# Optimization experiments

Hardware: AMD Instinct MI355X
Metric: run time of the kernel (lower is better)

Reference implementation:

```python
import jax, jax.numpy as jnp
import numpy as np

EPS = 1e-8
NUM_HEADS = 8
SCALE = 25.0
SIM_THRESH = 0.75
BLOCK = 10  # per-frame proposal group size used by the zeroing mask


def _l2norm(x):
    return x / (jnp.linalg.norm(x, axis=-1, keepdims=True) + EPS)


def setup_inputs() -> dict:
    key = jax.random.key(0)
    ks = jax.random.split(key, 7)
    B, N, C = 1, 2000, 256
    H = NUM_HEADS
    x_cls = jax.random.normal(ks[0], (B, N, C), dtype=jnp.float32)
    x_reg = jax.random.normal(ks[1], (B, N, C), dtype=jnp.float32)
    cls_score = jax.random.uniform(ks[2], (N,), dtype=jnp.float32)
    fg_score = jax.random.uniform(ks[3], (N,), dtype=jnp.float32)
    coord_attn = jax.random.uniform(ks[4], (B, H, N, N), dtype=jnp.float32)
    W_qkv_cls = jax.random.normal(ks[5], (3 * C, C), dtype=jnp.float32) * 0.02
    W_qkv_reg = jax.random.normal(ks[6], (3 * C, C), dtype=jnp.float32) * 0.02
    return {"x_cls": x_cls, "x_reg": x_reg, "cls_score": cls_score,
            "fg_score": fg_score, "coord_attn": coord_attn,
            "W_qkv_cls": W_qkv_cls, "W_qkv_reg": W_qkv_reg}


def reference(x_cls, x_reg, cls_score, fg_score, coord_attn, W_qkv_cls, W_qkv_reg):
    B, N, C = x_cls.shape
    H = NUM_HEADS
    D = C // H

    def qkv(x, W):
        t = (x @ W.T).reshape(B, N, 3, H, D).transpose(2, 0, 3, 1, 4)  # [3,B,H,N,D]
        return t[0], t[1], t[2]

    q_cls, k_cls, v_cls = qkv(x_cls, W_qkv_cls)
    q_reg, k_reg, v_reg = qkv(x_reg, W_qkv_reg)

    q_cls, k_cls = _l2norm(q_cls), _l2norm(k_cls)
    q_reg, k_reg = _l2norm(q_reg), _l2norm(k_reg)
    v_cls_normed = _l2norm(v_cls)

    cs = cls_score.reshape(1, 1, 1, N)  # broadcast over [B,H,N,N]
    fs = fg_score.reshape(1, 1, 1, N)

    attn_cls_raw = jnp.einsum('bhnd,bhmd->bhnm', v_cls_normed, v_cls_normed)

    attn_cls = jax.nn.softmax(jnp.einsum('bhnd,bhmd->bhnm', q_cls, k_cls) * SCALE * cs, axis=-1)
    attn_reg = jax.nn.softmax(jnp.einsum('bhnd,bhmd->bhnm', q_reg, k_reg) * SCALE * fs, axis=-1)

    attn = (attn_reg + attn_cls) * 0.5 * coord_attn
    attn = jax.lax.stop_gradient(attn)  # original detaches before masking

    # block-diagonal zeroing: row j zeros cols [j//10*10, j//10*10+9), keep diagonal
    rows = jnp.arange(N)[:, None]
    cols = jnp.arange(N)[None, :]
    block_start = (rows // BLOCK) * BLOCK
    zero_mask = (cols >= block_start) & (cols < block_start + (BLOCK - 1)) & (cols != rows)
    attn = jnp.where(zero_mask, 0.0, attn)

    x = jnp.einsum('bhnm,bhmd->bhnd', attn, v_cls).transpose(0, 2, 1, 3).reshape(B, N, C)
    x_ori = v_cls.transpose(0, 2, 1, 3).reshape(B, N, C)
    x_cat = jnp.concatenate([x, x_ori], axis=-1)  # [B,N,2C]

    # ave=True branch
    sim_raw = jnp.sum(attn_cls_raw, axis=1)[0] / H          # [N,N]
    sim_mask = (sim_raw > SIM_THRESH).astype(x_cls.dtype)
    sim_attn = jnp.sum(attn, axis=1)[0] / H                 # [N,N]
    sim_round2 = jax.nn.softmax(sim_attn, axis=-1)
    sim_round2 = sim_mask * sim_round2 / (jnp.sum(sim_mask * sim_round2, axis=-1, keepdims=True) + EPS)
    return x_cat, sim_round2
```

## Files before the change

### kernel.cpp

```cpp
#include <hip/hip_runtime.h>
#include <math.h>

typedef _Float16 half8 __attribute__((ext_vector_type(8)));
typedef _Float16 half4 __attribute__((ext_vector_type(4)));
typedef _Float16 half2v __attribute__((ext_vector_type(2)));
typedef float f32x4 __attribute__((ext_vector_type(4)));

constexpr int N = 2000;
constexpr int NP = 2048;
constexpr int H = 8;
constexpr int D = 32;
constexpr float SCL = 25.0f;
constexpr float L2E = 1.4426950408889634f;
constexpr float FM2 = 25.0f * L2E;

#define MFMA16(a,b,c)  __builtin_amdgcn_mfma_f32_16x16x32_f16((a),(b),(c),0,0,0)
#define MFMA16K(a,b,c) __builtin_amdgcn_mfma_f32_16x16x16f16((a),(b),(c),0,0,0)

__device__ __forceinline__ float fexp2(float x) { return __builtin_amdgcn_exp2f(x); }


__global__ __launch_bounds__(256) void wconv_kernel(
    const float* __restrict__ Wc, const float* __restrict__ Wr,
    _Float16* __restrict__ Wch, _Float16* __restrict__ Wrh)
{
    const int i = blockIdx.x * 256 + threadIdx.x;
    Wch[i] = (_Float16)Wc[i];
    Wrh[i] = (_Float16)Wr[i];
}

__global__ __launch_bounds__(256) void qkv_kernel(
    const float* __restrict__ xc, const float* __restrict__ xr,
    const _Float16* __restrict__ Wch, const _Float16* __restrict__ Wrh,
    const float* __restrict__ clsScore, const float* __restrict__ fgScore,
    _Float16* __restrict__ Qch, _Float16* __restrict__ Kch,
    _Float16* __restrict__ Qrh, _Float16* __restrict__ Krh,
    _Float16* __restrict__ Vnh, _Float16* __restrict__ Vth,
    float* __restrict__ out)
{
    constexpr int XS = 264;
    __shared__ _Float16 xs[16 * XS];
    const int t = threadIdx.x;
    const int n0 = blockIdx.x * 16;
    const int by = blockIdx.y;
    const int which = (by < 3) ? by : (by - 3);
    const bool isCls = by < 3;
    const float* x = isCls ? xc : xr;
    const _Float16* Wh = isCls ? Wch : Wrh;

    #pragma unroll
    for (int it = 0; it < 4; ++it) {
        const int f = t + it * 256;
        const int row = f >> 6, c4 = f & 63;
        const float4 v = *(const float4*)(x + (size_t)(n0 + row) * 256 + c4 * 4);
        half4 hv; hv[0]=(_Float16)v.x; hv[1]=(_Float16)v.y; hv[2]=(_Float16)v.z; hv[3]=(_Float16)v.w;
        *(half4*)&xs[row * XS + c4 * 4] = hv;
    }
    __syncthreads();

    const int w = t >> 6, l = t & 63;
    const int lr = l & 15, lg = l >> 4;
    const int obase = which * 256 + w * 64;
    f32x4 acc[4] = {{0,0,0,0},{0,0,0,0},{0,0,0,0},{0,0,0,0}};
    for (int k0 = 0; k0 < 256; k0 += 32) {
        const half8 aX = *(const half8*)&xs[lr * XS + k0 + lg * 8];
        #pragma unroll
        for (int s = 0; s < 4; ++s) {
            const half8 bW = *(const half8*)(Wh + (size_t)(obase + s * 16 + lr) * 256 + k0 + lg * 8);
            acc[s] = MFMA16(aX, bW, acc[s]);
        }
    }
    f32x4 kscale = {1.f,1.f,1.f,1.f};
    if (which == 1) {
        const float* sp = isCls ? clsScore : fgScore;
        kscale = (SCL * L2E) * *(const f32x4*)(sp + n0 + lg*4);
    }
    #pragma unroll
    for (int p = 0; p < 2; ++p) {
        const int h = 2 * w + p;
        float ss[4];
        #pragma unroll
        for (int j = 0; j < 4; ++j) {
            float v = acc[2*p][j]*acc[2*p][j] + acc[2*p+1][j]*acc[2*p+1][j];
            #pragma unroll
            for (int off = 1; off < 16; off <<= 1) v += __shfl_xor(v, off);
            ss[j] = sqrtf(v) + 1e-8f;
        }
        if (which < 2) {
            _Float16* Qd = isCls ? (which == 0 ? Qch : Kch) : (which == 0 ? Qrh : Krh);
            #pragma unroll
            for (int sh = 0; sh < 2; ++sh)
                #pragma unroll
                for (int j = 0; j < 4; ++j)
                    Qd[((size_t)h*NP + n0 + lg*4 + j)*D + sh*16 + lr]
                        = (_Float16)(acc[2*p+sh][j] / ss[j] * kscale[j]);
        } else {
            #pragma unroll
            for (int sh = 0; sh < 2; ++sh) {
                const int d = sh * 16 + lr;
                half4 tv;
                #pragma unroll
                for (int j = 0; j < 4; ++j) {
                    const float raw = acc[2*p+sh][j];
                    Vnh[((size_t)h*NP + n0 + lg*4 + j)*D + d] = (_Float16)(raw / ss[j]);
                    out[(size_t)(n0 + lg*4 + j)*512 + 256 + h*D + d] = raw;
                    tv[j] = (_Float16)raw;
                }
                *(half4*)(Vth + ((size_t)h*D + d)*NP + n0 + lg*4) = tv;
            }
        }
    }
}

__global__ __launch_bounds__(512) void stats_kernel(
    const _Float16* __restrict__ Qch, const _Float16* __restrict__ Kch,
    const _Float16* __restrict__ Qrh, const _Float16* __restrict__ Krh,
    float* __restrict__ BIAS)
{
    __shared__ float Ssh[2][4][16];
    const int t = threadIdx.x;
    const int w = t >> 6, l = t & 63;
    const int nsub = w >> 2, mq = w & 3;
    const int n0 = blockIdx.x * 32 + nsub * 16;
    const int h = blockIdx.y, z = blockIdx.z;
    const _Float16* Q = z ? Qrh : Qch;
    const _Float16* K = z ? Krh : Kch;
    const int lr = l & 15, lg = l >> 4;
    const half8 aQ = *(const half8*)(Q + ((size_t)h*NP + n0 + lr)*D + lg*8);
    float S[4] = {0.f, 0.f, 0.f, 0.f};
    const int mqB0 = (mq == 0) ? 0 : 31*mq;
    const int mqB1 = (mq == 3) ? 125 : 31*(mq+1);
    half8 bK = *(const half8*)(K + ((size_t)h*NP + mqB0*16 + lr)*D + lg*8);
    for (int ms = mqB0; ms < mqB1; ++ms) {
        const half8 cur = bK;
        if (ms + 1 < mqB1)
            bK = *(const half8*)(K + ((size_t)h*NP + (ms+1)*16 + lr)*D + lg*8);
        f32x4 z4 = {0.f, 0.f, 0.f, 0.f};
        const f32x4 c = MFMA16(aQ, cur, z4);
        #pragma unroll
        for (int j = 0; j < 4; ++j) S[j] += fexp2(c[j] - FM2);
    }
    #pragma unroll
    for (int j = 0; j < 4; ++j) {
        #pragma unroll
        for (int off = 1; off < 16; off <<= 1) S[j] += __shfl_xor(S[j], off);
    }
    if (lr == 0) {
        #pragma unroll
        for (int j = 0; j < 4; ++j) Ssh[nsub][mq][lg*4 + j] = S[j];
    }
    __syncthreads();
    if (t < 32) {
        const int ns = t >> 4, rl = t & 15;
        const int n = blockIdx.x * 32 + ns*16 + rl;
        BIAS[((size_t)z*H + h)*NP + n]
            = -__log2f(Ssh[ns][0][rl] + Ssh[ns][1][rl] + Ssh[ns][2][rl] + Ssh[ns][3][rl]) - FM2 - 1.0f;
    }
}

__global__ __launch_bounds__(256) void vvmask_kernel(
    const _Float16* __restrict__ Vnh, unsigned char* __restrict__ Mask)
{
    const int t = threadIdx.x;
    const int w = t >> 6, l = t & 63;
    const int n0 = blockIdx.y * 16;
    const int m00 = blockIdx.x * 256 + w * 64;
    const int lr = l & 15, lg = l >> 4;
    half8 aV[8];
    #pragma unroll
    for (int h = 0; h < 8; ++h)
        aV[h] = *(const half8*)(Vnh + ((size_t)(h*NP + n0 + lr))*D + lg*8);
    for (int s = 0; s < 4; ++s) {
        const int mb = m00 + s*16;
        f32x4 acc = {0.f, 0.f, 0.f, 0.f};
        #pragma unroll
        for (int h = 0; h < 8; ++h) {
            const half8 bV = *(const half8*)(Vnh + ((size_t)(h*NP + mb + lr))*D + lg*8);
            acc = MFMA16(aV[h], bV, acc);
        }
        const int m = mb + lr;
        if (m < N) {
            #pragma unroll
            for (int j = 0; j < 4; ++j) {
                const int n = n0 + lg*4 + j;
                Mask[(size_t)n*N + m] = (acc[j]*0.125f > 0.75f) ? (unsigned char)1 : (unsigned char)0;
            }
        }
    }
}

template<int SMAX>
__global__ __launch_bounds__(256) void attn_kernel(
    const _Float16* __restrict__ Kch, const _Float16* __restrict__ Krh,
    const _Float16* __restrict__ Qch, const _Float16* __restrict__ Qrh,
    const _Float16* __restrict__ Vth, const float* __restrict__ coord,
    const float* __restrict__ BIAS,
    _Float16* __restrict__ SIMH, _Float16* __restrict__ XPH, int mcBase)
{
    __shared__ _Float16 simred[4][16][SMAX*16 + 8];

    const int t = threadIdx.x;
    const int w = t >> 6, l = t & 63;
    const int lr = l & 15, lg = l >> 4;
    const int mc = mcBase + blockIdx.x;
    const int m0 = mc * 128;
    const int n0 = blockIdx.y * 16;
    const int n = n0 + lr;
    const int bs = (n / 10) * 10;
    const int h0 = 2 * w;

    unsigned kill = 0u;
    #pragma unroll
    for (int s = 0; s < SMAX; ++s)
        #pragma unroll
        for (int j = 0; j < 4; ++j) {
            const int m = m0 + s*16 + lg*4 + j;
            if (m >= bs && m < bs + 9 && m != n) kill |= (1u << (s*4 + j));
        }

    half2v sacc[SMAX][2];
    #pragma unroll
    for (int s = 0; s < SMAX; ++s)
        #pragma unroll
        for (int k = 0; k < 2; ++k) { sacc[s][k][0] = (_Float16)0.f; sacc[s][k][1] = (_Float16)0.f; }

    constexpr int NG = (SMAX + 3) / 4;

    #pragma unroll
    for (int hp = 0; hp < 2; ++hp) {
        const int h = h0 + hp;
        const half8 aQc = *(const half8*)(Qch + ((size_t)h*NP + n)*D + lg*8);
        const half8 aQr = *(const half8*)(Qrh + ((size_t)h*NP + n)*D + lg*8);
        const float bC = BIAS[(size_t)h*NP + n];
        const float bR = BIAS[(size_t)(H + h)*NP + n];
        f32x4 pv0 = {0,0,0,0}, pv1 = {0,0,0,0};

        #pragma unroll
        for (int g = 0; g < NG; ++g) {
            constexpr int GSfull = 4;
            const int gs = (SMAX - 4*g >= 4) ? GSfull : (SMAX - 4*g);
            half8 kc[4], kr[4]; half4 v0[4], v1[4]; f32x4 co[4];
            #pragma unroll
            for (int i = 0; i < 4; ++i) {
                if (i >= gs) break;
                const int s = 4*g + i;
                const int m = m0 + s*16;
                const size_t kb = ((size_t)h*NP + m + lr)*D + lg*8;
                kc[i] = *(const half8*)(Kch + kb);
                kr[i] = *(const half8*)(Krh + kb);
                v0[i] = *(const half4*)(Vth + ((size_t)(h*D + lr))*NP + m + lg*4);
                v1[i] = *(const half4*)(Vth + ((size_t)(h*D + 16 + lr))*NP + m + lg*4);
                co[i] = *(const f32x4*)(coord + ((size_t)h*N + n)*N + m + lg*4);
            }
            __builtin_amdgcn_sched_barrier(0);
            #pragma unroll
            for (int i = 0; i < 4; ++i) {
                if (i >= gs) break;
                const int s = 4*g + i;
                f32x4 z4 = {0,0,0,0};
                const f32x4 cc = MFMA16(kc[i], aQc, z4);
                const f32x4 cr = MFMA16(kr[i], aQr, z4);
                half4 af;
                #pragma unroll
                for (int j = 0; j < 4; ++j) {
                    float a = (fexp2(cc[j] + bC) + fexp2(cr[j] + bR)) * co[i][j];
                    if ((kill >> (s*4 + j)) & 1u) a = 0.f;
                    af[j] = (_Float16)a;
                }
                sacc[s][0] += (half2v){af[0], af[1]};
                sacc[s][1] += (half2v){af[2], af[3]};
                pv0 = MFMA16K(af, v0[i], pv0);
                pv1 = MFMA16K(af, v1[i], pv1);
            }
            __builtin_amdgcn_sched_barrier(0);
        }
        _Float16* xp = XPH + (((size_t)(mc*H + h)*N + n0 + lg*4))*D + lr;
        #pragma unroll
        for (int j = 0; j < 4; ++j) {
            xp[j*D]      = (_Float16)pv0[j];
            xp[j*D + 16] = (_Float16)pv1[j];
        }
    }

    #pragma unroll
    for (int s = 0; s < SMAX; ++s) {
        half4 sv; sv[0]=sacc[s][0][0]; sv[1]=sacc[s][0][1]; sv[2]=sacc[s][1][0]; sv[3]=sacc[s][1][1];
        *(half4*)&simred[w][lr][s*16 + lg*4] = sv;
    }
    __syncthreads();
    constexpr int C8 = SMAX * 2;
    for (int e = t; e < 16 * C8; e += 256) {
        const int r = e / C8, c8 = e % C8;
        const half8 s0 = *(const half8*)&simred[0][r][c8*8];
        const half8 s1 = *(const half8*)&simred[1][r][c8*8];
        const half8 s2 = *(const half8*)&simred[2][r][c8*8];
        const half8 s3 = *(const half8*)&simred[3][r][c8*8];
        const half8 sum = (s0 + s1) + (s2 + s3);
        *(half8*)(SIMH + (size_t)(n0 + r)*N + m0 + c8*8) = sum;
    }
}

__global__ __launch_bounds__(256) void reduce_kernel(
    const _Float16* __restrict__ XPH, float* __restrict__ out)
{
    const int n = blockIdx.x, t = threadIdx.x;
    const int h = t >> 5, d = t & 31;
    float acc = 0.f;
    #pragma unroll
    for (int mcI = 0; mcI < 16; ++mcI)
        acc += (float)XPH[(((size_t)mcI*H + h)*N + n)*D + d];
    out[(size_t)n*512 + t] = acc;
}

__global__ __launch_bounds__(256) void simfinal_kernel(
    const _Float16* __restrict__ SIMH, const unsigned char* __restrict__ Mask,
    float* __restrict__ out)
{
    __shared__ float redA[4], redB[4];
    const int n = blockIdx.x, t = threadIdx.x;
    const _Float16* row = SIMH + (size_t)n * N;
    const unsigned char* mrow = Mask + (size_t)n * N;
    const bool act = t < 250;
    float f[8];
    unsigned int mk0 = 0, mk1 = 0;
    float mx = -1e30f;
    if (act) {
        const half8 v8 = *(const half8*)(row + t*8);
        const uint2 mm = *(const uint2*)(mrow + t*8);
        mk0 = mm.x; mk1 = mm.y;
        #pragma unroll
        for (int k = 0; k < 8; ++k) { f[k] = (float)v8[k]; mx = fmaxf(mx, f[k]); }
    }
    #pragma unroll
    for (int off = 1; off < 64; off <<= 1) mx = fmaxf(mx, __shfl_xor(mx, off));
    const int wv = t >> 6;
    if ((t & 63) == 0) redA[wv] = mx;
    __syncthreads();
    const float M = fmaxf(fmaxf(redA[0], redA[1]), fmaxf(redA[2], redA[3]));
    float e[8];
    float sA = 0.f, sM = 0.f;
    if (act) {
        #pragma unroll
        for (int k = 0; k < 8; ++k) {
            e[k] = fexp2((f[k] - M) * (L2E * 0.125f));
            sA += e[k];
            const unsigned int mkb = ((k < 4 ? mk0 : mk1) >> (8*(k & 3))) & 0xffu;
            if (mkb) sM += e[k]; else e[k] = 0.f;
        }
    }
    #pragma unroll
    for (int off = 1; off < 64; off <<= 1) { sA += __shfl_xor(sA, off); sM += __shfl_xor(sM, off); }
    __syncthreads();
    if ((t & 63) == 0) { redA[wv] = sA; redB[wv] = sM; }
    __syncthreads();
    const float SA = redA[0] + redA[1] + redA[2] + redA[3];
    const float SMK = redB[0] + redB[1] + redB[2] + redB[3];
    const float inv = 1.f / (SMK + 1e-8f * SA);
    if (act) {
        float* orow = out + 1024000 + (size_t)n*N + t*8;
        *(float4*)(orow)     = make_float4(e[0]*inv, e[1]*inv, e[2]*inv, e[3]*inv);
        *(float4*)(orow + 4) = make_float4(e[4]*inv, e[5]*inv, e[6]*inv, e[7]*inv);
    }
}

extern "C" void kernel_launch(void* const* d_in, const int* in_sizes, int n_in,
                              void* d_out, int out_size, void* d_ws, size_t ws_size,
                              hipStream_t stream) {
    const float* x_cls     = (const float*)d_in[0];
    const float* x_reg     = (const float*)d_in[1];
    const float* cls_score = (const float*)d_in[2];
    const float* fg_score  = (const float*)d_in[3];
    const float* coord     = (const float*)d_in[4];
    const float* Wc        = (const float*)d_in[5];
    const float* Wr        = (const float*)d_in[6];

    char* base = (char*)d_ws;
    float* BIAS     = (float*)base;
    _Float16* SIMH  = (_Float16*)(base + 131072);
    _Float16* XPH   = (_Float16*)(base + 8131072);
    _Float16* Qch   = (_Float16*)(base + 24515072);
    _Float16* Kch   = Qch + 524288;
    _Float16* Qrh   = Qch + 2*524288;
    _Float16* Krh   = Qch + 3*524288;
    _Float16* Vnh   = Qch + 4*524288;
    _Float16* Vth   = Qch + 5*524288;
    _Float16* Wch   = (_Float16*)(base + 30806528);
    _Float16* Wrh   = (_Float16*)(base + 31199744);
    unsigned char* Mask = (unsigned char*)(base + 31592960);
    float* out = (float*)d_out;

    wconv_kernel<<<768, 256, 0, stream>>>(Wc, Wr, Wch, Wrh);
    qkv_kernel<<<dim3(125, 5), 256, 0, stream>>>(x_cls, x_reg, Wch, Wrh, cls_score, fg_score,
                                                 Qch, Kch, Qrh, Krh, Vnh, Vth, out);
    stats_kernel<<<dim3(63, 8, 2), 512, 0, stream>>>(Qch, Kch, Qrh, Krh, BIAS);
    vvmask_kernel<<<dim3(8, 125), 256, 0, stream>>>(Vnh, Mask);
    attn_kernel<8><<<dim3(15, 125), 256, 0, stream>>>(Kch, Krh, Qch, Qrh, Vth, coord,
                                                      BIAS, SIMH, XPH, 0);
    attn_kernel<5><<<dim3(1, 125), 256, 0, stream>>>(Kch, Krh, Qch, Qrh, Vth, coord,
                                                     BIAS, SIMH, XPH, 15);
    reduce_kernel<<<2000, 256, 0, stream>>>(XPH, out);
    simfinal_kernel<<<2000, 256, 0, stream>>>(SIMH, Mask, out);
}
```

Measured before the change: 135.2 us.

## Prepack coord attention into fp16 MFMA-fragment layout before attention

Adds a kernel that converts the coord_attn tensor to fp16 and stores it tiled in the exact per-lane fragment order used by the attention kernel. The attention kernel then loads contiguous half4 values instead of strided fp32 rows, aiming to improve coalescing and halve bytes in the hot loop. This adds an extra full pass over the large coord tensor plus a 64MB intermediate write and read, and reduces coord precision to fp16.

```diff
diff --git a/kernel.cpp b/kernel.cpp
--- a/kernel.cpp
+++ b/kernel.cpp
@@ -27,6 +27,35 @@
     const int i = blockIdx.x * 256 + threadIdx.x;
     Wch[i] = (_Float16)Wc[i];
     Wrh[i] = (_Float16)Wr[i];
+}
+
+__global__ __launch_bounds__(256) void pack_kernel(
+    const float* __restrict__ coord, _Float16* __restrict__ CH)
+{
+    const int ny = blockIdx.x, h = blockIdx.y;
+    const int t = threadIdx.x;
+    const int row = t >> 4;
+    const int c0 = (t & 15) * 4;
+    const float* src = coord + ((size_t)h*N + ny*16 + row)*N;
+    _Float16* dstbase = CH + ((size_t)(h*125 + ny))*125*256;
+    const int lp = ((t & 3) << 4) | row;
+    #pragma unroll 8
+    for (int k = 0; k < 31; ++k) {
+        const int colb = c0 + 64*k;
+        const f32x4 v = *(const f32x4*)(src + colb);
+        const int ms = colb >> 4;
+        half4 hv; hv[0]=(_Float16)v[0]; hv[1]=(_Float16)v[1]; hv[2]=(_Float16)v[2]; hv[3]=(_Float16)v[3];
+        *(half4*)(dstbase + ((size_t)ms*64 + lp)*4) = hv;
+    }
+    {
+        const int colb = c0 + 64*31;
+        if (colb < 2000) {
+            const f32x4 v = *(const f32x4*)(src + colb);
+            const int ms = colb >> 4;
+            half4 hv; hv[0]=(_Float16)v[0]; hv[1]=(_Float16)v[1]; hv[2]=(_Float16)v[2]; hv[3]=(_Float16)v[3];
+            *(half4*)(dstbase + ((size_t)ms*64 + lp)*4) = hv;
+        }
+    }
 }
 
 __global__ __launch_bounds__(256) void qkv_kernel(
@@ -193,7 +222,7 @@
 __global__ __launch_bounds__(256) void attn_kernel(
     const _Float16* __restrict__ Kch, const _Float16* __restrict__ Krh,
     const _Float16* __restrict__ Qch, const _Float16* __restrict__ Qrh,
-    const _Float16* __restrict__ Vth, const float* __restrict__ coord,
+    const _Float16* __restrict__ Vth, const _Float16* __restrict__ CH,
     const float* __restrict__ BIAS,
     _Float16* __restrict__ SIMH, _Float16* __restrict__ XPH, int mcBase)
 {
@@ -203,8 +232,9 @@
     const int w = t >> 6, l = t & 63;
     const int lr = l & 15, lg = l >> 4;
     const int mc = mcBase + blockIdx.x;
+    const int ny = blockIdx.y;
     const int m0 = mc * 128;
-    const int n0 = blockIdx.y * 16;
+    const int n0 = ny * 16;
     const int n = n0 + lr;
     const int bs = (n / 10) * 10;
     const int h0 = 2 * w;
@@ -233,13 +263,14 @@
         const half8 aQr = *(const half8*)(Qrh + ((size_t)h*NP + n)*D + lg*8);
         const float bC = BIAS[(size_t)h*NP + n];
         const float bR = BIAS[(size_t)(H + h)*NP + n];
+        const _Float16* chh = CH + ((size_t)(h*125 + ny)*125 + mc*8)*256;
         f32x4 pv0 = {0,0,0,0}, pv1 = {0,0,0,0};
 
         #pragma unroll
         for (int g = 0; g < NG; ++g) {
             constexpr int GSfull = 4;
             const int gs = (SMAX - 4*g >= 4) ? GSfull : (SMAX - 4*g);
-            half8 kc[4], kr[4]; half4 v0[4], v1[4]; f32x4 co[4];
+            half8 kc[4], kr[4]; half4 v0[4], v1[4], co[4];
             #pragma unroll
             for (int i = 0; i < 4; ++i) {
                 if (i >= gs) break;
@@ -250,7 +281,7 @@
                 kr[i] = *(const half8*)(Krh + kb);
                 v0[i] = *(const half4*)(Vth + ((size_t)(h*D + lr))*NP + m + lg*4);
                 v1[i] = *(const half4*)(Vth + ((size_t)(h*D + 16 + lr))*NP + m + lg*4);
-                co[i] = *(const f32x4*)(coord + ((size_t)h*N + n)*N + m + lg*4);
+                co[i] = *(const half4*)(chh + s*256 + l*4);
             }
             __builtin_amdgcn_sched_barrier(0);
             #pragma unroll
@@ -263,7 +294,7 @@
                 half4 af;
                 #pragma unroll
                 for (int j = 0; j < 4; ++j) {
-                    float a = (fexp2(cc[j] + bC) + fexp2(cr[j] + bR)) * co[i][j];
+                    float a = (fexp2(cc[j] + bC) + fexp2(cr[j] + bR)) * (float)co[i][j];
                     if ((kill >> (s*4 + j)) & 1u) a = 0.f;
                     af[j] = (_Float16)a;
                 }
@@ -387,16 +418,18 @@
     _Float16* Wch   = (_Float16*)(base + 30806528);
     _Float16* Wrh   = (_Float16*)(base + 31199744);
     unsigned char* Mask = (unsigned char*)(base + 31592960);
+    _Float16* CH    = (_Float16*)(base + 35592960);
     float* out = (float*)d_out;
 
     wconv_kernel<<<768, 256, 0, stream>>>(Wc, Wr, Wch, Wrh);
+    pack_kernel<<<dim3(125, 8), 256, 0, stream>>>(coord, CH);
     qkv_kernel<<<dim3(125, 5), 256, 0, stream>>>(x_cls, x_reg, Wch, Wrh, cls_score, fg_score,
                                                  Qch, Kch, Qrh, Krh, Vnh, Vth, out);
     stats_kernel<<<dim3(63, 8, 2), 512, 0, stream>>>(Qch, Kch, Qrh, Krh, BIAS);
     vvmask_kernel<<<dim3(8, 125), 256, 0, stream>>>(Vnh, Mask);
-    attn_kernel<8><<<dim3(15, 125), 256, 0, stream>>>(Kch, Krh, Qch, Qrh, Vth, coord,
+    attn_kernel<8><<<dim3(15, 125), 256, 0, stream>>>(Kch, Krh, Qch, Qrh, Vth, CH,
                                                       BIAS, SIMH, XPH, 0);
-    attn_kernel<5><<<dim3(1, 125), 256, 0, stream>>>(Kch, Krh, Qch, Qrh, Vth, coord,
+    attn_kernel<5><<<dim3(1, 125), 256, 0, stream>>>(Kch, Krh, Qch, Qrh, Vth, CH,
                                                      BIAS, SIMH, XPH, 15);
     reduce_kernel<<<2000, 256, 0, stream>>>(XPH, out);
     simfinal_kernel<<<2000, 256, 0, stream>>>(SIMH, Mask, out);
```

New measurement: 159.1 us. 17.8% more time.

## Split fused attention into score, coord-stream, and PV kernels via fp16 buffer

Applied to the files above, without the earlier changes.

The fused attention kernel is split into three passes. The first computes exp scores into an fp16 [H,N,N] buffer. The second streams coord_attn with that buffer, applies the block mask, writes the masked probabilities back and produces the head-summed similarity. The third runs the P·V matmul per head and writes the output directly, which removes the per-chunk partial buffer and its reduce kernel. This makes the coord read fully coalesced and separates the memory-bound and compute-bound work. The cost is writing and re-reading a 64 MB fp16 intermediate twice more.

```diff
diff --git a/kernel.cpp b/kernel.cpp
--- a/kernel.cpp
+++ b/kernel.cpp
@@ -3,7 +3,6 @@
 
 typedef _Float16 half8 __attribute__((ext_vector_type(8)));
 typedef _Float16 half4 __attribute__((ext_vector_type(4)));
-typedef _Float16 half2v __attribute__((ext_vector_type(2)));
 typedef float f32x4 __attribute__((ext_vector_type(4)));
 
 constexpr int N = 2000;
@@ -190,15 +189,11 @@
 }
 
 template<int SMAX>
-__global__ __launch_bounds__(256) void attn_kernel(
+__global__ __launch_bounds__(256) void escore_kernel(
     const _Float16* __restrict__ Kch, const _Float16* __restrict__ Krh,
     const _Float16* __restrict__ Qch, const _Float16* __restrict__ Qrh,
-    const _Float16* __restrict__ Vth, const float* __restrict__ coord,
-    const float* __restrict__ BIAS,
-    _Float16* __restrict__ SIMH, _Float16* __restrict__ XPH, int mcBase)
-{
-    __shared__ _Float16 simred[4][16][SMAX*16 + 8];
-
+    const float* __restrict__ BIAS, _Float16* __restrict__ EP, int mcBase)
+{
     const int t = threadIdx.x;
     const int w = t >> 6, l = t & 63;
     const int lr = l & 15, lg = l >> 4;
@@ -206,23 +201,7 @@
     const int m0 = mc * 128;
     const int n0 = blockIdx.y * 16;
     const int n = n0 + lr;
-    const int bs = (n / 10) * 10;
     const int h0 = 2 * w;
-
-    unsigned kill = 0u;
-    #pragma unroll
-    for (int s = 0; s < SMAX; ++s)
-        #pragma unroll
-        for (int j = 0; j < 4; ++j) {
-            const int m = m0 + s*16 + lg*4 + j;
-            if (m >= bs && m < bs + 9 && m != n) kill |= (1u << (s*4 + j));
-        }
-
-    half2v sacc[SMAX][2];
-    #pragma unroll
-    for (int s = 0; s < SMAX; ++s)
-        #pragma unroll
-        for (int k = 0; k < 2; ++k) { sacc[s][k][0] = (_Float16)0.f; sacc[s][k][1] = (_Float16)0.f; }
 
     constexpr int NG = (SMAX + 3) / 4;
 
@@ -233,24 +212,19 @@
         const half8 aQr = *(const half8*)(Qrh + ((size_t)h*NP + n)*D + lg*8);
         const float bC = BIAS[(size_t)h*NP + n];
         const float bR = BIAS[(size_t)(H + h)*NP + n];
-        f32x4 pv0 = {0,0,0,0}, pv1 = {0,0,0,0};
+        _Float16* erow = EP + ((size_t)h*N + n)*N;
 
         #pragma unroll
         for (int g = 0; g < NG; ++g) {
-            constexpr int GSfull = 4;
-            const int gs = (SMAX - 4*g >= 4) ? GSfull : (SMAX - 4*g);
-            half8 kc[4], kr[4]; half4 v0[4], v1[4]; f32x4 co[4];
+            const int gs = (SMAX - 4*g >= 4) ? 4 : (SMAX - 4*g);
+            half8 kc[4], kr[4];
             #pragma unroll
             for (int i = 0; i < 4; ++i) {
                 if (i >= gs) break;
                 const int s = 4*g + i;
-                const int m = m0 + s*16;
-                const size_t kb = ((size_t)h*NP + m + lr)*D + lg*8;
+                const size_t kb = ((size_t)h*NP + m0 + s*16 + lr)*D + lg*8;
                 kc[i] = *(const half8*)(Kch + kb);
                 kr[i] = *(const half8*)(Krh + kb);
-                v0[i] = *(const half4*)(Vth + ((size_t)(h*D + lr))*NP + m + lg*4);
-                v1[i] = *(const half4*)(Vth + ((size_t)(h*D + 16 + lr))*NP + m + lg*4);
-                co[i] = *(const f32x4*)(coord + ((size_t)h*N + n)*N + m + lg*4);
             }
             __builtin_amdgcn_sched_barrier(0);
             #pragma unroll
@@ -260,56 +234,106 @@
                 f32x4 z4 = {0,0,0,0};
                 const f32x4 cc = MFMA16(kc[i], aQc, z4);
                 const f32x4 cr = MFMA16(kr[i], aQr, z4);
-                half4 af;
+                half4 ev;
                 #pragma unroll
-                for (int j = 0; j < 4; ++j) {
-                    float a = (fexp2(cc[j] + bC) + fexp2(cr[j] + bR)) * co[i][j];
-                    if ((kill >> (s*4 + j)) & 1u) a = 0.f;
-                    af[j] = (_Float16)a;
-                }
-                sacc[s][0] += (half2v){af[0], af[1]};
-                sacc[s][1] += (half2v){af[2], af[3]};
-                pv0 = MFMA16K(af, v0[i], pv0);
-                pv1 = MFMA16K(af, v1[i], pv1);
+                for (int j = 0; j < 4; ++j)
+                    ev[j] = (_Float16)(fexp2(cc[j] + bC) + fexp2(cr[j] + bR));
+                *(half4*)(erow + m0 + s*16 + lg*4) = ev;
             }
-            __builtin_amdgcn_sched_barrier(0);
-        }
-        _Float16* xp = XPH + (((size_t)(mc*H + h)*N + n0 + lg*4))*D + lr;
-        #pragma unroll
-        for (int j = 0; j < 4; ++j) {
-            xp[j*D]      = (_Float16)pv0[j];
-            xp[j*D + 16] = (_Float16)pv1[j];
-        }
-    }
-
-    #pragma unroll
-    for (int s = 0; s < SMAX; ++s) {
-        half4 sv; sv[0]=sacc[s][0][0]; sv[1]=sacc[s][0][1]; sv[2]=sacc[s][1][0]; sv[3]=sacc[s][1][1];
-        *(half4*)&simred[w][lr][s*16 + lg*4] = sv;
-    }
-    __syncthreads();
-    constexpr int C8 = SMAX * 2;
-    for (int e = t; e < 16 * C8; e += 256) {
-        const int r = e / C8, c8 = e % C8;
-        const half8 s0 = *(const half8*)&simred[0][r][c8*8];
-        const half8 s1 = *(const half8*)&simred[1][r][c8*8];
-        const half8 s2 = *(const half8*)&simred[2][r][c8*8];
-        const half8 s3 = *(const half8*)&simred[3][r][c8*8];
-        const half8 sum = (s0 + s1) + (s2 + s3);
-        *(half8*)(SIMH + (size_t)(n0 + r)*N + m0 + c8*8) = sum;
-    }
-}
-
-__global__ __launch_bounds__(256) void reduce_kernel(
-    const _Float16* __restrict__ XPH, float* __restrict__ out)
-{
-    const int n = blockIdx.x, t = threadIdx.x;
-    const int h = t >> 5, d = t & 31;
-    float acc = 0.f;
-    #pragma unroll
-    for (int mcI = 0; mcI < 16; ++mcI)
-        acc += (float)XPH[(((size_t)mcI*H + h)*N + n)*D + d];
-    out[(size_t)n*512 + t] = acc;
+        }
+    }
+}
+
+__global__ __launch_bounds__(256) void stream_kernel(
+    const float* __restrict__ coord, _Float16* __restrict__ EP,
+    _Float16* __restrict__ SIMH)
+{
+    constexpr int GTOT = N * (N / 4);
+    for (int g = blockIdx.x * 256 + threadIdx.x; g < GTOT; g += gridDim.x * 256) {
+        const int n = g / (N / 4);
+        const int m = (g - n * (N / 4)) * 4;
+        const int bs = (n / 10) * 10;
+        f32x4 s4 = {0.f, 0.f, 0.f, 0.f};
+        #pragma unroll
+        for (int h = 0; h < 8; ++h) {
+            const size_t off = ((size_t)h*N + n)*N + m;
+            const f32x4 co = *(const f32x4*)(coord + off);
+            const half4 e = *(const half4*)(EP + off);
+            half4 p;
+            #pragma unroll
+            for (int j = 0; j < 4; ++j) {
+                const int mm = m + j;
+                float a = (float)e[j] * co[j];
+                if (mm >= bs && mm < bs + 9 && mm != n) a = 0.f;
+                p[j] = (_Float16)a;
+                s4[j] += a;
+            }
+            *(half4*)(EP + off) = p;
+        }
+        half4 sv;
+        #pragma unroll
+        for (int j = 0; j < 4; ++j) sv[j] = (_Float16)s4[j];
+        *(half4*)(SIMH + (size_t)n*N + m) = sv;
+    }
+}
+
+__global__ __launch_bounds__(256) void pv_kernel(
+    const _Float16* __restrict__ EP, const _Float16* __restrict__ Vth,
+    float* __restrict__ out)
+{
+    __shared__ _Float16 pvred[4][2][16][18];
+    const int t = threadIdx.x;
+    const int w = t >> 6, l = t & 63;
+    const int lr = l & 15, lg = l >> 4;
+    const int n0 = blockIdx.x * 16;
+    const int h  = blockIdx.y;
+    const int n  = n0 + lr;
+
+    const _Float16* prow = EP + ((size_t)h*N + n)*N;
+    const _Float16* v0row = Vth + ((size_t)(h*D + lr))*NP;
+    const _Float16* v1row = Vth + ((size_t)(h*D + 16 + lr))*NP;
+
+    f32x4 aA0 = {0,0,0,0}, aA1 = {0,0,0,0}, aB0 = {0,0,0,0}, aB1 = {0,0,0,0};
+    for (int ms = w; ms < 125; ms += 8) {
+        const int m1 = ms*16;
+        const int ms2 = ms + 4;
+        const half4 afA = *(const half4*)(prow + m1 + lg*4);
+        const half4 v0A = *(const half4*)(v0row + m1 + lg*4);
+        const half4 v1A = *(const half4*)(v1row + m1 + lg*4);
+        half4 afB{}, v0B{}, v1B{};
+        if (ms2 < 125) {
+            const int m2 = ms2*16;
+            afB = *(const half4*)(prow + m2 + lg*4);
+            v0B = *(const half4*)(v0row + m2 + lg*4);
+            v1B = *(const half4*)(v1row + m2 + lg*4);
+        }
+        __builtin_amdgcn_sched_barrier(0);
+        aA0 = MFMA16K(afA, v0A, aA0);
+        aA1 = MFMA16K(afA, v1A, aA1);
+        if (ms2 < 125) {
+            aB0 = MFMA16K(afB, v0B, aB0);
+            aB1 = MFMA16K(afB, v1B, aB1);
+        }
+    }
+    const f32x4 pv0 = aA0 + aB0;
+    const f32x4 pv1 = aA1 + aB1;
+    {
+        half4 h0v, h1v;
+        #pragma unroll
+        for (int j = 0; j < 4; ++j) { h0v[j] = (_Float16)pv0[j]; h1v[j] = (_Float16)pv1[j]; }
+        *(half4*)&pvred[w][0][lr][lg*4] = h0v;
+        *(half4*)&pvred[w][1][lr][lg*4] = h1v;
+    }
+    __syncthreads();
+    {
+        const int e0 = 2*t;
+        const int d = e0 & 15, db = (e0 >> 4) & 1, q = e0 >> 5;
+        const float u0 = (float)pvred[0][db][d][q]   + (float)pvred[1][db][d][q]
+                       + (float)pvred[2][db][d][q]   + (float)pvred[3][db][d][q];
+        const float u1 = (float)pvred[0][db][d+1][q] + (float)pvred[1][db][d+1][q]
+                       + (float)pvred[2][db][d+1][q] + (float)pvred[3][db][d+1][q];
+        *(float2*)(out + (size_t)(n0 + q)*512 + h*32 + db*16 + d) = make_float2(u0, u1);
+    }
 }
 
 __global__ __launch_bounds__(256) void simfinal_kernel(
@@ -377,16 +401,16 @@
     char* base = (char*)d_ws;
     float* BIAS     = (float*)base;
     _Float16* SIMH  = (_Float16*)(base + 131072);
-    _Float16* XPH   = (_Float16*)(base + 8131072);
-    _Float16* Qch   = (_Float16*)(base + 24515072);
+    _Float16* EP    = (_Float16*)(base + 8131072);
+    _Float16* Qch   = (_Float16*)(base + 72131072);
     _Float16* Kch   = Qch + 524288;
     _Float16* Qrh   = Qch + 2*524288;
     _Float16* Krh   = Qch + 3*524288;
     _Float16* Vnh   = Qch + 4*524288;
     _Float16* Vth   = Qch + 5*524288;
-    _Float16* Wch   = (_Float16*)(base + 30806528);
-    _Float16* Wrh   = (_Float16*)(base + 31199744);
-    unsigned char* Mask = (unsigned char*)(base + 31592960);
+    _Float16* Wch   = (_Float16*)(base + 78422528);
+    _Float16* Wrh   = (_Float16*)(base + 78815744);
+    unsigned char* Mask = (unsigned char*)(base + 79208960);
     float* out = (float*)d_out;
 
     wconv_kernel<<<768, 256, 0, stream>>>(Wc, Wr, Wch, Wrh);
@@ -394,10 +418,9 @@
                                                  Qch, Kch, Qrh, Krh, Vnh, Vth, out);
     stats_kernel<<<dim3(63, 8, 2), 512, 0, stream>>>(Qch, Kch, Qrh, Krh, BIAS);
     vvmask_kernel<<<dim3(8, 125), 256, 0, stream>>>(Vnh, Mask);
-    attn_kernel<8><<<dim3(15, 125), 256, 0, stream>>>(Kch, Krh, Qch, Qrh, Vth, coord,
-                                                      BIAS, SIMH, XPH, 0);
-    attn_kernel<5><<<dim3(1, 125), 256, 0, stream>>>(Kch, Krh, Qch, Qrh, Vth, coord,
-                                                     BIAS, SIMH, XPH, 15);
-    reduce_kernel<<<2000, 256, 0, stream>>>(XPH, out);
+    escore_kernel<8><<<dim3(15, 125), 256, 0, stream>>>(Kch, Krh, Qch, Qrh, BIAS, EP, 0);
+    escore_kernel<5><<<dim3(1, 125), 256, 0, stream>>>(Kch, Krh, Qch, Qrh, BIAS, EP, 15);
+    stream_kernel<<<2048, 256, 0, stream>>>(coord, EP, SIMH);
+    pv_kernel<<<dim3(125, 8), 256, 0, stream>>>(EP, Vth, out);
     simfinal_kernel<<<2000, 256, 0, stream>>>(SIMH, Mask, out);
 }
```

Measured after the change: 165.8 us. 22.7% more time.

## Restructure attention to one block per head and row tile, staging coord in LDS

Applied to the files above, without the earlier changes.

The attention kernel now assigns one block per (head, 16-row tile) and loops over all 2000 columns, so partial PV results are reduced inside the block through LDS. This removes the XPH partial buffer and the separate reduce kernel. The coord tile is prefetched into double-buffered shared memory for coalesced loads. The per-head attention weights are no longer summed across heads in registers; each head writes its own fp16 slice to an 8x larger SIM buffer that simfinal then sums. This trades the cross-head reduction for a much larger global write and read, and the launch grid shrinks to 1000 blocks.

```diff
diff --git a/kernel.cpp b/kernel.cpp
--- a/kernel.cpp
+++ b/kernel.cpp
@@ -3,7 +3,6 @@
 
 typedef _Float16 half8 __attribute__((ext_vector_type(8)));
 typedef _Float16 half4 __attribute__((ext_vector_type(4)));
-typedef _Float16 half2v __attribute__((ext_vector_type(2)));
 typedef float f32x4 __attribute__((ext_vector_type(4)));
 
 constexpr int N = 2000;
@@ -189,147 +188,146 @@
     }
 }
 
-template<int SMAX>
 __global__ __launch_bounds__(256) void attn_kernel(
     const _Float16* __restrict__ Kch, const _Float16* __restrict__ Krh,
     const _Float16* __restrict__ Qch, const _Float16* __restrict__ Qrh,
     const _Float16* __restrict__ Vth, const float* __restrict__ coord,
     const float* __restrict__ BIAS,
-    _Float16* __restrict__ SIMH, _Float16* __restrict__ XPH, int mcBase)
-{
-    __shared__ _Float16 simred[4][16][SMAX*16 + 8];
+    _Float16* __restrict__ SIMH8, float* __restrict__ out)
+{
+    constexpr int CW = 264;
+    __shared__ float costage[2][16][CW];
+    __shared__ float pvred[4][2][16][17];
 
     const int t = threadIdx.x;
     const int w = t >> 6, l = t & 63;
     const int lr = l & 15, lg = l >> 4;
-    const int mc = mcBase + blockIdx.x;
-    const int m0 = mc * 128;
-    const int n0 = blockIdx.y * 16;
-    const int n = n0 + lr;
+    const int h  = blockIdx.x;
+    const int ny = blockIdx.y;
+    const int n0 = ny * 16;
+    const int n  = n0 + lr;
     const int bs = (n / 10) * 10;
-    const int h0 = 2 * w;
-
-    unsigned kill = 0u;
-    #pragma unroll
-    for (int s = 0; s < SMAX; ++s)
-        #pragma unroll
-        for (int j = 0; j < 4; ++j) {
-            const int m = m0 + s*16 + lg*4 + j;
-            if (m >= bs && m < bs + 9 && m != n) kill |= (1u << (s*4 + j));
-        }
-
-    half2v sacc[SMAX][2];
-    #pragma unroll
-    for (int s = 0; s < SMAX; ++s)
-        #pragma unroll
-        for (int k = 0; k < 2; ++k) { sacc[s][k][0] = (_Float16)0.f; sacc[s][k][1] = (_Float16)0.f; }
-
-    constexpr int NG = (SMAX + 3) / 4;
-
-    #pragma unroll
-    for (int hp = 0; hp < 2; ++hp) {
-        const int h = h0 + hp;
-        const half8 aQc = *(const half8*)(Qch + ((size_t)h*NP + n)*D + lg*8);
-        const half8 aQr = *(const half8*)(Qrh + ((size_t)h*NP + n)*D + lg*8);
-        const float bC = BIAS[(size_t)h*NP + n];
-        const float bR = BIAS[(size_t)(H + h)*NP + n];
-        f32x4 pv0 = {0,0,0,0}, pv1 = {0,0,0,0};
-
-        #pragma unroll
-        for (int g = 0; g < NG; ++g) {
-            constexpr int GSfull = 4;
-            const int gs = (SMAX - 4*g >= 4) ? GSfull : (SMAX - 4*g);
-            half8 kc[4], kr[4]; half4 v0[4], v1[4]; f32x4 co[4];
-            #pragma unroll
-            for (int i = 0; i < 4; ++i) {
-                if (i >= gs) break;
-                const int s = 4*g + i;
-                const int m = m0 + s*16;
-                const size_t kb = ((size_t)h*NP + m + lr)*D + lg*8;
-                kc[i] = *(const half8*)(Kch + kb);
-                kr[i] = *(const half8*)(Krh + kb);
-                v0[i] = *(const half4*)(Vth + ((size_t)(h*D + lr))*NP + m + lg*4);
-                v1[i] = *(const half4*)(Vth + ((size_t)(h*D + 16 + lr))*NP + m + lg*4);
-                co[i] = *(const f32x4*)(coord + ((size_t)h*N + n)*N + m + lg*4);
+
+    const half8 aQc = *(const half8*)(Qch + ((size_t)h*NP + n)*D + lg*8);
+    const half8 aQr = *(const half8*)(Qrh + ((size_t)h*NP + n)*D + lg*8);
+    const float bC = BIAS[(size_t)h*NP + n];
+    const float bR = BIAS[(size_t)(H + h)*NP + n];
+
+    f32x4 streg[4];
+    auto LOADCH = [&](int c) {
+        #pragma unroll
+        for (int i = 0; i < 4; ++i) {
+            const int g = t + 256*i;
+            const int row = g >> 6, c4 = g & 63;
+            const int col = c*256 + c4*4;
+            if (col < 2000)
+                streg[i] = *(const f32x4*)(coord + ((size_t)h*N + n0 + row)*N + col);
+            else
+                streg[i] = (f32x4){0.f,0.f,0.f,0.f};
+        }
+    };
+    auto WRITECH = [&](int buf) {
+        #pragma unroll
+        for (int i = 0; i < 4; ++i) {
+            const int g = t + 256*i;
+            const int row = g >> 6, c4 = g & 63;
+            *(f32x4*)&costage[buf][row][c4*4] = streg[i];
+        }
+    };
+
+    f32x4 pv0 = {0,0,0,0}, pv1 = {0,0,0,0};
+
+    LOADCH(0);
+    WRITECH(0);
+    __syncthreads();
+    int buf = 0;
+
+    for (int c = 0; c < 8; ++c) {
+        const bool more = (c + 1 < 8);
+        if (more) LOADCH(c + 1);
+        __builtin_amdgcn_sched_barrier(0);
+
+        const int nls = (c < 7) ? 4 : ((w < 3) ? 4 : 1);
+
+        half8 kc[4], kr[4]; half4 v0[4], v1[4];
+        #pragma unroll
+        for (int i = 0; i < 4; ++i) {
+            if (i >= nls) break;
+            const int s = c*16 + w*4 + i;
+            const int m = s*16;
+            const size_t kb = ((size_t)h*NP + m + lr)*D + lg*8;
+            kc[i] = *(const half8*)(Kch + kb);
+            kr[i] = *(const half8*)(Krh + kb);
+            v0[i] = *(const half4*)(Vth + ((size_t)(h*D + lr))*NP + m + lg*4);
+            v1[i] = *(const half4*)(Vth + ((size_t)(h*D + 16 + lr))*NP + m + lg*4);
+        }
+        __builtin_amdgcn_sched_barrier(0);
+
+        #pragma unroll
+        for (int i = 0; i < 4; ++i) {
+            if (i >= nls) break;
+            const int s = c*16 + w*4 + i;
+            const f32x4 co = *(const f32x4*)&costage[buf][lr][(w*4 + i)*16 + lg*4];
+            f32x4 z4 = {0,0,0,0};
+            const f32x4 cc = MFMA16(kc[i], aQc, z4);
+            const f32x4 cr = MFMA16(kr[i], aQr, z4);
+            half4 af;
+            #pragma unroll
+            for (int j = 0; j < 4; ++j) {
+                const int m = s*16 + lg*4 + j;
+                float a = (fexp2(cc[j] + bC) + fexp2(cr[j] + bR)) * co[j];
+                if (m >= bs && m < bs + 9 && m != n) a = 0.f;
+                af[j] = (_Float16)a;
             }
-            __builtin_amdgcn_sched_barrier(0);
-            #pragma unroll
-            for (int i = 0; i < 4; ++i) {
-                if (i >= gs) break;
-                const int s = 4*g + i;
-                f32x4 z4 = {0,0,0,0};
-                const f32x4 cc = MFMA16(kc[i], aQc, z4);
-                const f32x4 cr = MFMA16(kr[i], aQr, z4);
-                half4 af;
-                #pragma unroll
-                for (int j = 0; j < 4; ++j) {
-                    float a = (fexp2(cc[j] + bC) + fexp2(cr[j] + bR)) * co[i][j];
-                    if ((kill >> (s*4 + j)) & 1u) a = 0.f;
-                    af[j] = (_Float16)a;
-                }
-                sacc[s][0] += (half2v){af[0], af[1]};
-                sacc[s][1] += (half2v){af[2], af[3]};
-                pv0 = MFMA16K(af, v0[i], pv0);
-                pv1 = MFMA16K(af, v1[i], pv1);
-            }
-            __builtin_amdgcn_sched_barrier(0);
-        }
-        _Float16* xp = XPH + (((size_t)(mc*H + h)*N + n0 + lg*4))*D + lr;
-        #pragma unroll
-        for (int j = 0; j < 4; ++j) {
-            xp[j*D]      = (_Float16)pv0[j];
-            xp[j*D + 16] = (_Float16)pv1[j];
-        }
-    }
-
-    #pragma unroll
-    for (int s = 0; s < SMAX; ++s) {
-        half4 sv; sv[0]=sacc[s][0][0]; sv[1]=sacc[s][0][1]; sv[2]=sacc[s][1][0]; sv[3]=sacc[s][1][1];
-        *(half4*)&simred[w][lr][s*16 + lg*4] = sv;
-    }
-    __syncthreads();
-    constexpr int C8 = SMAX * 2;
-    for (int e = t; e < 16 * C8; e += 256) {
-        const int r = e / C8, c8 = e % C8;
-        const half8 s0 = *(const half8*)&simred[0][r][c8*8];
-        const half8 s1 = *(const half8*)&simred[1][r][c8*8];
-        const half8 s2 = *(const half8*)&simred[2][r][c8*8];
-        const half8 s3 = *(const half8*)&simred[3][r][c8*8];
-        const half8 sum = (s0 + s1) + (s2 + s3);
-        *(half8*)(SIMH + (size_t)(n0 + r)*N + m0 + c8*8) = sum;
-    }
-}
-
-__global__ __launch_bounds__(256) void reduce_kernel(
-    const _Float16* __restrict__ XPH, float* __restrict__ out)
-{
-    const int n = blockIdx.x, t = threadIdx.x;
-    const int h = t >> 5, d = t & 31;
-    float acc = 0.f;
-    #pragma unroll
-    for (int mcI = 0; mcI < 16; ++mcI)
-        acc += (float)XPH[(((size_t)mcI*H + h)*N + n)*D + d];
-    out[(size_t)n*512 + t] = acc;
+            *(half4*)(SIMH8 + ((size_t)h*N + n)*N + s*16 + lg*4) = af;
+            pv0 = MFMA16K(af, v0[i], pv0);
+            pv1 = MFMA16K(af, v1[i], pv1);
+        }
+
+        if (more) WRITECH(buf ^ 1);
+        __syncthreads();
+        buf ^= 1;
+    }
+
+    #pragma unroll
+    for (int j = 0; j < 4; ++j) {
+        pvred[w][0][lr][lg*4 + j] = pv0[j];
+        pvred[w][1][lr][lg*4 + j] = pv1[j];
+    }
+    __syncthreads();
+    {
+        const int e0 = 2*t;
+        const int d = e0 & 15, db = (e0 >> 4) & 1, q = e0 >> 5;
+        const float u0 = pvred[0][db][d][q]   + pvred[1][db][d][q]
+                       + pvred[2][db][d][q]   + pvred[3][db][d][q];
+        const float u1 = pvred[0][db][d+1][q] + pvred[1][db][d+1][q]
+                       + pvred[2][db][d+1][q] + pvred[3][db][d+1][q];
+        *(float2*)(out + (size_t)(n0 + q)*512 + h*32 + db*16 + d) = make_float2(u0, u1);
+    }
 }
 
 __global__ __launch_bounds__(256) void simfinal_kernel(
-    const _Float16* __restrict__ SIMH, const unsigned char* __restrict__ Mask,
+    const _Float16* __restrict__ SIMH8, const unsigned char* __restrict__ Mask,
     float* __restrict__ out)
 {
     __shared__ float redA[4], redB[4];
     const int n = blockIdx.x, t = threadIdx.x;
-    const _Float16* row = SIMH + (size_t)n * N;
     const unsigned char* mrow = Mask + (size_t)n * N;
     const bool act = t < 250;
-    float f[8];
+    float f[8] = {0,0,0,0,0,0,0,0};
     unsigned int mk0 = 0, mk1 = 0;
     float mx = -1e30f;
     if (act) {
-        const half8 v8 = *(const half8*)(row + t*8);
+        #pragma unroll
+        for (int h = 0; h < 8; ++h) {
+            const half8 v8 = *(const half8*)(SIMH8 + ((size_t)h*N + n)*N + t*8);
+            #pragma unroll
+            for (int k = 0; k < 8; ++k) f[k] += (float)v8[k];
+        }
         const uint2 mm = *(const uint2*)(mrow + t*8);
         mk0 = mm.x; mk1 = mm.y;
         #pragma unroll
-        for (int k = 0; k < 8; ++k) { f[k] = (float)v8[k]; mx = fmaxf(mx, f[k]); }
+        for (int k = 0; k < 8; ++k) mx = fmaxf(mx, f[k]);
     }
     #pragma unroll
     for (int off = 1; off < 64; off <<= 1) mx = fmaxf(mx, __shfl_xor(mx, off));
@@ -375,18 +373,17 @@
     const float* Wr        = (const float*)d_in[6];
 
     char* base = (char*)d_ws;
-    float* BIAS     = (float*)base;
-    _Float16* SIMH  = (_Float16*)(base + 131072);
-    _Float16* XPH   = (_Float16*)(base + 8131072);
-    _Float16* Qch   = (_Float16*)(base + 24515072);
-    _Float16* Kch   = Qch + 524288;
-    _Float16* Qrh   = Qch + 2*524288;
-    _Float16* Krh   = Qch + 3*524288;
-    _Float16* Vnh   = Qch + 4*524288;
-    _Float16* Vth   = Qch + 5*524288;
-    _Float16* Wch   = (_Float16*)(base + 30806528);
-    _Float16* Wrh   = (_Float16*)(base + 31199744);
-    unsigned char* Mask = (unsigned char*)(base + 31592960);
+    float* BIAS      = (float*)base;
+    _Float16* SIMH8  = (_Float16*)(base + 131072);
+    _Float16* Qch    = (_Float16*)(base + 64131072);
+    _Float16* Kch    = Qch + 524288;
+    _Float16* Qrh    = Qch + 2*524288;
+    _Float16* Krh    = Qch + 3*524288;
+    _Float16* Vnh    = Qch + 4*524288;
+    _Float16* Vth    = Qch + 5*524288;
+    _Float16* Wch    = (_Float16*)(base + 70422528);
+    _Float16* Wrh    = (_Float16*)(base + 70815744);
+    unsigned char* Mask = (unsigned char*)(base + 71208960);
     float* out = (float*)d_out;
 
     wconv_kernel<<<768, 256, 0, stream>>>(Wc, Wr, Wch, Wrh);
@@ -394,10 +391,7 @@
                                                  Qch, Kch, Qrh, Krh, Vnh, Vth, out);
     stats_kernel<<<dim3(63, 8, 2), 512, 0, stream>>>(Qch, Kch, Qrh, Krh, BIAS);
     vvmask_kernel<<<dim3(8, 125), 256, 0, stream>>>(Vnh, Mask);
-    attn_kernel<8><<<dim3(15, 125), 256, 0, stream>>>(Kch, Krh, Qch, Qrh, Vth, coord,
-                                                      BIAS, SIMH, XPH, 0);
-    attn_kernel<5><<<dim3(1, 125), 256, 0, stream>>>(Kch, Krh, Qch, Qrh, Vth, coord,
-                                                     BIAS, SIMH, XPH, 15);
-    reduce_kernel<<<2000, 256, 0, stream>>>(XPH, out);
-    simfinal_kernel<<<2000, 256, 0, stream>>>(SIMH, Mask, out);
-}
+    attn_kernel<<<dim3(8, 125), 256, 0, stream>>>(Kch, Krh, Qch, Qrh, Vth, coord,
+                                                  BIAS, SIMH8, out);
+    simfinal_kernel<<<2000, 256, 0, stream>>>(SIMH8, Mask, out);
+}
```

Result: faster. 132.1 us (-2.3%).
